# Kernel tuning notes

Measured on AMD Instinct MI355X. Metric: run time of the kernel, lower is better.

The kernel has to match this reference:

```python
import jax, jax.numpy as jnp
import numpy as np

MARGIN = 0.2


def colbert_score(q, d):
    # q: (B, Q, D), d: (B, K, D) -> scalar
    sim = jnp.einsum('bqd,bkd->bqk', q, d)          # (B, Q, K)
    max_sim = jnp.max(sim, axis=2)                   # (B, Q) row-wise max over doc tokens
    return jnp.sum(max_sim)                          # sum over query tokens and batch


def setup_inputs() -> dict:
    key = jax.random.key(0)
    k1, k2, k3 = jax.random.split(key, 3)
    B, Q, K, D = 256, 256, 512, 128
    return {
        'q': jax.random.normal(k1, (B, Q, D), dtype=jnp.float32),
        'p': jax.random.normal(k2, (B, K, D), dtype=jnp.float32),
        'n': jax.random.normal(k3, (B, K, D), dtype=jnp.float32),
    }


def reference(q, p, n):
    pos_score = colbert_score(q, p)
    neg_score = colbert_score(q, n)
    loss = jax.nn.relu(MARGIN + neg_score - pos_score)
    # torch .mean() on a scalar is identity
    return loss
```

## Files before the change

kernel.cpp:

```cpp
#include <hip/hip_runtime.h>


#define MARGIN   0.2f
#define Bn       256
#define Qn       256
#define Kn       512
#define Dn       128
#define TN       32
#define NT       (Kn / TN)
#define BSTR     136
#define NTHREADS 256

typedef __attribute__((ext_vector_type(8))) short short8;
typedef __attribute__((ext_vector_type(4))) short short4v;
typedef __attribute__((ext_vector_type(4))) float f32x4;

__device__ __forceinline__ unsigned short f2bf(float x) {
    unsigned int u = __float_as_uint(x);
    return (unsigned short)((u + 0x7FFFu + ((u >> 16) & 1u)) >> 16);
}
__device__ __forceinline__ float bf2f(unsigned short h) {
    return __uint_as_float(((unsigned int)h) << 16);
}

__global__ __launch_bounds__(NTHREADS, 1)
void colbert_mfma_kernel(const float* __restrict__ qg,
                         const float* __restrict__ pg,
                         const float* __restrict__ ng,
                         float* __restrict__ sum_ws) {
    __shared__ short Bs[2][2][TN * BSTR];
    __shared__ float part[4];

    const int tid  = threadIdx.x;
    const int w    = tid >> 6;
    const int lane = tid & 63;
    const int l16  = lane & 15;
    const int quad = lane >> 4;
    const int b    = blockIdx.x;

    short8 Ahi[4][4], Alo[4][4];
    {
        const float* qb = qg + (size_t)b * Qn * Dn;
#pragma unroll
        for (int mi = 0; mi < 4; ++mi)
#pragma unroll
            for (int ks = 0; ks < 4; ++ks) {
                const float* src = qb + (size_t)(w * 64 + mi * 16 + l16) * Dn
                                      + ks * 32 + quad * 8;
                float4 v0 = *(const float4*)src;
                float4 v1 = *(const float4*)(src + 4);
                float x[8] = {v0.x, v0.y, v0.z, v0.w, v1.x, v1.y, v1.z, v1.w};
#pragma unroll
                for (int j = 0; j < 8; ++j) {
                    unsigned short h = f2bf(x[j]);
                    Ahi[mi][ks][j] = (short)h;
                    Alo[mi][ks][j] = (short)f2bf(x[j] - bf2f(h));
                }
            }
    }

    float maxp[4][4], maxn[4][4];
#pragma unroll
    for (int mi = 0; mi < 4; ++mi)
#pragma unroll
        for (int r = 0; r < 4; ++r) { maxp[mi][r] = -3e38f; maxn[mi][r] = -3e38f; }

    const float* dbase0 = pg + (size_t)b * Kn * Dn;
    const float* dbase1 = ng + (size_t)b * Kn * Dn;

    float4 pre[4];
    {
        const float4* s4 = (const float4*)dbase0;
#pragma unroll
        for (int k = 0; k < 4; ++k) pre[k] = s4[tid + 256 * k];
    }

    int buf = 0;
    for (int t = 0; t < 2 * NT; ++t) {
#pragma unroll
        for (int k = 0; k < 4; ++k) {
            int i   = tid + 256 * k;
            int doc = i >> 5;
            int d4  = i & 31;
            float4 v = pre[k];
            float x[4] = {v.x, v.y, v.z, v.w};
            short4v hi, lo;
#pragma unroll
            for (int j = 0; j < 4; ++j) {
                unsigned short h = f2bf(x[j]);
                hi[j] = (short)h;
                lo[j] = (short)f2bf(x[j] - bf2f(h));
            }
            *(short4v*)&Bs[buf][0][doc * BSTR + d4 * 4] = hi;
            *(short4v*)&Bs[buf][1][doc * BSTR + d4 * 4] = lo;
        }
        __syncthreads();

        if (t + 1 < 2 * NT) {
            int tn = t + 1;
            const float* base = (tn < NT) ? dbase0 : dbase1;
            const float4* s4 = (const float4*)(base + (size_t)(tn & (NT - 1)) * TN * Dn);
#pragma unroll
            for (int k = 0; k < 4; ++k) pre[k] = s4[tid + 256 * k];
        }

        f32x4 acc[4][2];
#pragma unroll
        for (int mi = 0; mi < 4; ++mi)
#pragma unroll
            for (int ni = 0; ni < 2; ++ni) acc[mi][ni] = (f32x4){0.f, 0.f, 0.f, 0.f};

#pragma unroll
        for (int ni = 0; ni < 2; ++ni) {
            short8 bhi[4], blo[4];
#pragma unroll
            for (int ks = 0; ks < 4; ++ks) {
                int off = (ni * 16 + l16) * BSTR + ks * 32 + quad * 8;
                bhi[ks] = *(const short8*)&Bs[buf][0][off];
                blo[ks] = *(const short8*)&Bs[buf][1][off];
            }
#pragma unroll
            for (int ks = 0; ks < 4; ++ks)
#pragma unroll
                for (int mi = 0; mi < 4; ++mi) {
                    acc[mi][ni] = __builtin_amdgcn_mfma_f32_16x16x32_bf16(
                        Ahi[mi][ks], bhi[ks], acc[mi][ni], 0, 0, 0);
                    acc[mi][ni] = __builtin_amdgcn_mfma_f32_16x16x32_bf16(
                        Ahi[mi][ks], blo[ks], acc[mi][ni], 0, 0, 0);
                    acc[mi][ni] = __builtin_amdgcn_mfma_f32_16x16x32_bf16(
                        Alo[mi][ks], bhi[ks], acc[mi][ni], 0, 0, 0);
                }
        }

        if (t < NT) {
#pragma unroll
            for (int mi = 0; mi < 4; ++mi)
#pragma unroll
                for (int r = 0; r < 4; ++r)
                    maxp[mi][r] = fmaxf(maxp[mi][r], fmaxf(acc[mi][0][r], acc[mi][1][r]));
        } else {
#pragma unroll
            for (int mi = 0; mi < 4; ++mi)
#pragma unroll
                for (int r = 0; r < 4; ++r)
                    maxn[mi][r] = fmaxf(maxn[mi][r], fmaxf(acc[mi][0][r], acc[mi][1][r]));
        }
        buf ^= 1;
    }

#pragma unroll
    for (int off = 1; off < 16; off <<= 1) {
#pragma unroll
        for (int mi = 0; mi < 4; ++mi)
#pragma unroll
            for (int r = 0; r < 4; ++r) {
                maxp[mi][r] = fmaxf(maxp[mi][r], __shfl_xor(maxp[mi][r], off));
                maxn[mi][r] = fmaxf(maxn[mi][r], __shfl_xor(maxn[mi][r], off));
            }
    }
    float s = 0.f;
#pragma unroll
    for (int mi = 0; mi < 4; ++mi)
#pragma unroll
        for (int r = 0; r < 4; ++r) s += maxp[mi][r] - maxn[mi][r];
    if (l16 != 0) s = 0.f;
    s += __shfl_xor(s, 16);
    s += __shfl_xor(s, 32);
    if (lane == 0) part[w] = s;
    __syncthreads();
    if (tid == 0)
        atomicAdd(sum_ws, part[0] + part[1] + part[2] + part[3]);
}

__global__ void finalize_kernel(const float* __restrict__ sum_ws,
                                float* __restrict__ out) {
    out[0] = fmaxf(0.0f, MARGIN - sum_ws[0]);
}

extern "C" void kernel_launch(void* const* d_in, const int* in_sizes, int n_in,
                              void* d_out, int out_size, void* d_ws, size_t ws_size,
                              hipStream_t stream) {
    const float* q = (const float*)d_in[0];
    const float* p = (const float*)d_in[1];
    const float* n = (const float*)d_in[2];
    float* out = (float*)d_out;
    float* ws  = (float*)d_ws;

    hipMemsetAsync(ws, 0, sizeof(float), stream);

    colbert_mfma_kernel<<<dim3(Bn), NTHREADS, 0, stream>>>(q, p, n, ws);
    finalize_kernel<<<1, 1, 0, stream>>>(ws, out);
}
```

Baseline: 188.8 us.

## Split positive and negative scoring into separate blocks and truncate bf16 split

Launches a 2D grid with one block per batch item and per document set (positive or negative), which doubles the block count so more CUs are busy. It also lets two blocks share a CU via launch bounds. The hi/lo bf16 split now uses truncation instead of round-to-nearest, which cuts ALU work in the conversion. MFMAs are regrouped by operand pair, and the result is accumulated as a signed double atomic. The cost is that query tiles are loaded and split twice, truncation loses some precision in the split, and the atomic becomes double precision.

```diff
diff --git a/kernel.cpp b/kernel.cpp
--- a/kernel.cpp
+++ b/kernel.cpp
@@ -15,19 +15,18 @@
 typedef __attribute__((ext_vector_type(4))) short short4v;
 typedef __attribute__((ext_vector_type(4))) float f32x4;
 
-__device__ __forceinline__ unsigned short f2bf(float x) {
+__device__ __forceinline__ void split_trunc(float x, unsigned short& hi, unsigned short& lo) {
     unsigned int u = __float_as_uint(x);
-    return (unsigned short)((u + 0x7FFFu + ((u >> 16) & 1u)) >> 16);
-}
-__device__ __forceinline__ float bf2f(unsigned short h) {
-    return __uint_as_float(((unsigned int)h) << 16);
+    hi = (unsigned short)(u >> 16);
+    float l = x - __uint_as_float(u & 0xFFFF0000u);
+    lo = (unsigned short)(__float_as_uint(l) >> 16);
 }
 
-__global__ __launch_bounds__(NTHREADS, 1)
-void colbert_mfma_kernel(const float* __restrict__ qg,
+__global__ __launch_bounds__(NTHREADS, 2)
+void colbert_pass_kernel(const float* __restrict__ qg,
                          const float* __restrict__ pg,
                          const float* __restrict__ ng,
-                         float* __restrict__ sum_ws) {
+                         double* __restrict__ sum_ws) {
     __shared__ short Bs[2][2][TN * BSTR];
     __shared__ float part[4];
 
@@ -37,6 +36,16 @@
     const int l16  = lane & 15;
     const int quad = lane >> 4;
     const int b    = blockIdx.x;
+    const int pass = blockIdx.y;
+
+    const float* docb = (pass ? ng : pg) + (size_t)b * Kn * Dn;
+
+    float4 pre[4];
+    {
+        const float4* s4 = (const float4*)docb;
+#pragma unroll
+        for (int k = 0; k < 4; ++k) pre[k] = s4[tid + 256 * k];
+    }
 
     short8 Ahi[4][4], Alo[4][4];
     {
@@ -52,31 +61,22 @@
                 float x[8] = {v0.x, v0.y, v0.z, v0.w, v1.x, v1.y, v1.z, v1.w};
 #pragma unroll
                 for (int j = 0; j < 8; ++j) {
-                    unsigned short h = f2bf(x[j]);
+                    unsigned short h, l;
+                    split_trunc(x[j], h, l);
                     Ahi[mi][ks][j] = (short)h;
-                    Alo[mi][ks][j] = (short)f2bf(x[j] - bf2f(h));
+                    Alo[mi][ks][j] = (short)l;
                 }
             }
     }
 
-    float maxp[4][4], maxn[4][4];
+    float maxv[4][4];
 #pragma unroll
     for (int mi = 0; mi < 4; ++mi)
 #pragma unroll
-        for (int r = 0; r < 4; ++r) { maxp[mi][r] = -3e38f; maxn[mi][r] = -3e38f; }
-
-    const float* dbase0 = pg + (size_t)b * Kn * Dn;
-    const float* dbase1 = ng + (size_t)b * Kn * Dn;
-
-    float4 pre[4];
-    {
-        const float4* s4 = (const float4*)dbase0;
-#pragma unroll
-        for (int k = 0; k < 4; ++k) pre[k] = s4[tid + 256 * k];
-    }
+        for (int r = 0; r < 4; ++r) maxv[mi][r] = -3e38f;
 
     int buf = 0;
-    for (int t = 0; t < 2 * NT; ++t) {
+    for (int t = 0; t < NT; ++t) {
 #pragma unroll
         for (int k = 0; k < 4; ++k) {
             int i   = tid + 256 * k;
@@ -87,19 +87,18 @@
             short4v hi, lo;
 #pragma unroll
             for (int j = 0; j < 4; ++j) {
-                unsigned short h = f2bf(x[j]);
+                unsigned short h, l;
+                split_trunc(x[j], h, l);
                 hi[j] = (short)h;
-                lo[j] = (short)f2bf(x[j] - bf2f(h));
+                lo[j] = (short)l;
             }
             *(short4v*)&Bs[buf][0][doc * BSTR + d4 * 4] = hi;
             *(short4v*)&Bs[buf][1][doc * BSTR + d4 * 4] = lo;
         }
         __syncthreads();
 
-        if (t + 1 < 2 * NT) {
-            int tn = t + 1;
-            const float* base = (tn < NT) ? dbase0 : dbase1;
-            const float4* s4 = (const float4*)(base + (size_t)(tn & (NT - 1)) * TN * Dn);
+        if (t + 1 < NT) {
+            const float4* s4 = (const float4*)(docb + (size_t)(t + 1) * TN * Dn);
 #pragma unroll
             for (int k = 0; k < 4; ++k) pre[k] = s4[tid + 256 * k];
         }
@@ -120,61 +119,57 @@
                 blo[ks] = *(const short8*)&Bs[buf][1][off];
             }
 #pragma unroll
-            for (int ks = 0; ks < 4; ++ks)
+            for (int ks = 0; ks < 4; ++ks) {
 #pragma unroll
-                for (int mi = 0; mi < 4; ++mi) {
+                for (int mi = 0; mi < 4; ++mi)
                     acc[mi][ni] = __builtin_amdgcn_mfma_f32_16x16x32_bf16(
                         Ahi[mi][ks], bhi[ks], acc[mi][ni], 0, 0, 0);
+#pragma unroll
+                for (int mi = 0; mi < 4; ++mi)
+                    acc[mi][ni] = __builtin_amdgcn_mfma_f32_16x16x32_bf16(
+                        Alo[mi][ks], bhi[ks], acc[mi][ni], 0, 0, 0);
+#pragma unroll
+                for (int mi = 0; mi < 4; ++mi)
                     acc[mi][ni] = __builtin_amdgcn_mfma_f32_16x16x32_bf16(
                         Ahi[mi][ks], blo[ks], acc[mi][ni], 0, 0, 0);
-                    acc[mi][ni] = __builtin_amdgcn_mfma_f32_16x16x32_bf16(
-                        Alo[mi][ks], bhi[ks], acc[mi][ni], 0, 0, 0);
-                }
+            }
         }
 
-        if (t < NT) {
 #pragma unroll
-            for (int mi = 0; mi < 4; ++mi)
+        for (int mi = 0; mi < 4; ++mi)
 #pragma unroll
-                for (int r = 0; r < 4; ++r)
-                    maxp[mi][r] = fmaxf(maxp[mi][r], fmaxf(acc[mi][0][r], acc[mi][1][r]));
-        } else {
-#pragma unroll
-            for (int mi = 0; mi < 4; ++mi)
-#pragma unroll
-                for (int r = 0; r < 4; ++r)
-                    maxn[mi][r] = fmaxf(maxn[mi][r], fmaxf(acc[mi][0][r], acc[mi][1][r]));
-        }
+            for (int r = 0; r < 4; ++r)
+                maxv[mi][r] = fmaxf(maxv[mi][r], fmaxf(acc[mi][0][r], acc[mi][1][r]));
         buf ^= 1;
     }
 
 #pragma unroll
-    for (int off = 1; off < 16; off <<= 1) {
+    for (int off = 1; off < 16; off <<= 1)
 #pragma unroll
         for (int mi = 0; mi < 4; ++mi)
 #pragma unroll
-            for (int r = 0; r < 4; ++r) {
-                maxp[mi][r] = fmaxf(maxp[mi][r], __shfl_xor(maxp[mi][r], off));
-                maxn[mi][r] = fmaxf(maxn[mi][r], __shfl_xor(maxn[mi][r], off));
-            }
-    }
+            for (int r = 0; r < 4; ++r)
+                maxv[mi][r] = fmaxf(maxv[mi][r], __shfl_xor(maxv[mi][r], off));
+
     float s = 0.f;
 #pragma unroll
     for (int mi = 0; mi < 4; ++mi)
 #pragma unroll
-        for (int r = 0; r < 4; ++r) s += maxp[mi][r] - maxn[mi][r];
+        for (int r = 0; r < 4; ++r) s += maxv[mi][r];
     if (l16 != 0) s = 0.f;
     s += __shfl_xor(s, 16);
     s += __shfl_xor(s, 32);
     if (lane == 0) part[w] = s;
     __syncthreads();
-    if (tid == 0)
-        atomicAdd(sum_ws, part[0] + part[1] + part[2] + part[3]);
+    if (tid == 0) {
+        double t = (double)part[0] + part[1] + part[2] + part[3];
+        atomicAdd(sum_ws, pass ? -t : t);
+    }
 }
 
-__global__ void finalize_kernel(const float* __restrict__ sum_ws,
+__global__ void finalize_kernel(const double* __restrict__ sum_ws,
                                 float* __restrict__ out) {
-    out[0] = fmaxf(0.0f, MARGIN - sum_ws[0]);
+    out[0] = fmaxf(0.0f, MARGIN - (float)sum_ws[0]);
 }
 
 extern "C" void kernel_launch(void* const* d_in, const int* in_sizes, int n_in,
@@ -184,10 +179,10 @@
     const float* p = (const float*)d_in[1];
     const float* n = (const float*)d_in[2];
     float* out = (float*)d_out;
-    float* ws  = (float*)d_ws;
+    double* ws = (double*)d_ws;
 
-    hipMemsetAsync(ws, 0, sizeof(float), stream);
+    hipMemsetAsync(ws, 0, sizeof(double), stream);
 
-    colbert_mfma_kernel<<<dim3(Bn), NTHREADS, 0, stream>>>(q, p, n, ws);
+    colbert_pass_kernel<<<dim3(Bn, 2), NTHREADS, 0, stream>>>(q, p, n, ws);
     finalize_kernel<<<1, 1, 0, stream>>>(ws, out);
 }
```

New measurement: 180.3 us. 1.05x faster.
